# Kernel tuning notes

Measured on AMD Instinct MI355X. Metric: run time of the kernel, lower is better.

The kernel has to match this reference:

```python
import jax, jax.numpy as jnp
import numpy as np

LOCAL_RADIUS = 5


def setup_inputs() -> dict:
    key = jax.random.key(0)
    k1, k2, k3 = jax.random.split(key, 3)
    B, K, C, H = 4, 4096, 256, 128
    x = jax.random.normal(k1, (B, K, C), dtype=jnp.float32)
    W1 = jax.random.normal(k2, (C, H), dtype=jnp.float32) * (1.0 / np.sqrt(C))
    b1 = jnp.zeros((H,), dtype=jnp.float32)
    W2 = jax.random.normal(k3, (H, 1), dtype=jnp.float32) * (1.0 / np.sqrt(H))
    b2 = jnp.zeros((1,), dtype=jnp.float32)
    return {"x": x, "W1": W1, "b1": b1, "W2": W2, "b2": b2}


def reference(x, W1, b1, W2, b2):
    # x: [B, k, C]. The MLP score for column j is independent of the row i,
    # so compute it once per token instead of per (i, window) as in the torch loop.
    B, k, C = x.shape
    s = (jnp.tanh(x @ W1 + b1) @ W2 + b2)[..., 0]  # [B, k]
    idx = jnp.arange(k)
    band = (jnp.abs(idx[:, None] - idx[None, :]) <= LOCAL_RADIUS)  # [k, k]
    # Outside the band the original leaves scores at 0.0 (not -inf), so
    # out-of-window positions still contribute exp(0)=1 to the softmax.
    scores = jnp.where(band[None, :, :], s[:, None, :], jnp.float32(0.0))  # [B, k, k]
    weights = jax.nn.softmax(scores, axis=-1)  # [B, k, k]
    weighted = jnp.einsum('bij,bjc->bic', weights, x)  # [B, k, C]
    return weighted, weights
```

## Files before the change

### kernel.cpp

```cpp
#include <hip/hip_runtime.h>
#include <math.h>

#define B_ 4
#define K_ 4096
#define C_ 256
#define H_ 128
#define RAD 5

typedef float floatx4 __attribute__((ext_vector_type(4)));


__global__ __launch_bounds__(128) void score_kernel(
    const float* __restrict__ x, const float* __restrict__ W1,
    const float* __restrict__ b1, const float* __restrict__ W2,
    const float* __restrict__ b2, float* __restrict__ s_out)
{
    const int tid = threadIdx.x;
    const int t0 = blockIdx.x * 8;
    const float* xr[8];
    #pragma unroll
    for (int t = 0; t < 8; ++t) xr[t] = x + (size_t)(t0 + t) * C_;

    float acc[8];
    float binit = b1[tid];
    #pragma unroll
    for (int t = 0; t < 8; ++t) acc[t] = binit;

    for (int c = 0; c < C_; c += 4) {
        float w0 = W1[(c + 0) * H_ + tid];
        float w1 = W1[(c + 1) * H_ + tid];
        float w2 = W1[(c + 2) * H_ + tid];
        float w3 = W1[(c + 3) * H_ + tid];
        #pragma unroll
        for (int t = 0; t < 8; ++t) {
            floatx4 xv = *(const floatx4*)&xr[t][c];
            acc[t] = fmaf(xv.x, w0, acc[t]);
            acc[t] = fmaf(xv.y, w1, acc[t]);
            acc[t] = fmaf(xv.z, w2, acc[t]);
            acc[t] = fmaf(xv.w, w3, acc[t]);
        }
    }

    __shared__ float red[2][8];
    float w2v = W2[tid];
    #pragma unroll
    for (int t = 0; t < 8; ++t) {
        float p = tanhf(acc[t]) * w2v;
        #pragma unroll
        for (int off = 32; off > 0; off >>= 1) p += __shfl_down(p, off);
        if ((tid & 63) == 0) red[tid >> 6][t] = p;
    }
    __syncthreads();
    if (tid < 8) s_out[t0 + tid] = red[0][tid] + red[1][tid] + b2[0];
}

__global__ __launch_bounds__(256) void colsum_partial(
    const float* __restrict__ x, float* __restrict__ partial)
{
    const int tid = threadIdx.x;
    const int blk = blockIdx.x;
    const float* base = x + (size_t)blk * 32 * C_ + tid;
    float a0 = 0.f, a1 = 0.f, a2 = 0.f, a3 = 0.f;
    #pragma unroll
    for (int kk = 0; kk < 32; kk += 4) {
        a0 += base[(size_t)(kk + 0) * C_];
        a1 += base[(size_t)(kk + 1) * C_];
        a2 += base[(size_t)(kk + 2) * C_];
        a3 += base[(size_t)(kk + 3) * C_];
    }
    partial[(size_t)blk * C_ + tid] = (a0 + a1) + (a2 + a3);
}

__global__ __launch_bounds__(256) void colsum_final(
    const float* __restrict__ partial, float* __restrict__ Ssum)
{
    const int tid = threadIdx.x;
    const int b = blockIdx.x;
    float acc = 0.f;
    for (int chunk = 0; chunk < 128; ++chunk)
        acc += partial[(size_t)(b * 128 + chunk) * C_ + tid];
    Ssum[b * C_ + tid] = acc;
}

__global__ __launch_bounds__(256) void attn_kernel(
    const float* __restrict__ x, const float* __restrict__ s,
    const float* __restrict__ Ssum, float* __restrict__ out)
{
    const int tid = threadIdx.x;
    const int blk = blockIdx.x;
    const int b = blk >> 12;
    const int i = blk & (K_ - 1);

    __shared__ float wb[2 * RAD + 1];
    __shared__ float woff_s;
    __shared__ int j0_s, j1_s;

    if (tid == 0) {
        int j0 = i - RAD; if (j0 < 0) j0 = 0;
        int j1 = i + RAD; if (j1 > K_ - 1) j1 = K_ - 1;
        int nb = j1 - j0 + 1;
        float sv[2 * RAD + 1];
        float m = 0.f;
        const float* srow = s + b * K_;
        for (int jj = 0; jj < nb; ++jj) {
            float v = srow[j0 + jj];
            sv[jj] = v;
            m = fmaxf(m, v);
        }
        float e0 = expf(-m);
        float D = (float)(K_ - nb) * e0;
        for (int jj = 0; jj < nb; ++jj) { float e = expf(sv[jj] - m); sv[jj] = e; D += e; }
        float inv = 1.0f / D;
        for (int jj = 0; jj < nb; ++jj) wb[jj] = sv[jj] * inv;
        woff_s = e0 * inv;
        j0_s = j0; j1_s = j1;
    }
    __syncthreads();
    const float woff = woff_s;
    const int j0 = j0_s, j1 = j1_s;

    floatx4* wrow4 = (floatx4*)(out + (size_t)B_ * K_ * C_ + (size_t)blk * K_);
    #pragma unroll
    for (int q = 0; q < 4; ++q) {
        const int f = tid + 256 * q;
        const int jb = f * 4;
        floatx4 v = { woff, woff, woff, woff };
        if (jb + 3 >= j0 && jb <= j1) {
            if (jb + 0 >= j0 && jb + 0 <= j1) v.x = wb[jb + 0 - j0];
            if (jb + 1 >= j0 && jb + 1 <= j1) v.y = wb[jb + 1 - j0];
            if (jb + 2 >= j0 && jb + 2 <= j1) v.z = wb[jb + 2 - j0];
            if (jb + 3 >= j0 && jb + 3 <= j1) v.w = wb[jb + 3 - j0];
        }
        __builtin_nontemporal_store(v, wrow4 + f);
    }

    {
        float acc = woff * Ssum[b * C_ + tid];
        const float* xb = x + ((size_t)b * K_) * C_ + tid;
        for (int j = j0; j <= j1; ++j)
            acc = fmaf(wb[j - j0] - woff, xb[(size_t)j * C_], acc);
        __builtin_nontemporal_store(acc, out + (size_t)blk * C_ + tid);
    }
}

extern "C" void kernel_launch(void* const* d_in, const int* in_sizes, int n_in,
                              void* d_out, int out_size, void* d_ws, size_t ws_size,
                              hipStream_t stream) {
    const float* x  = (const float*)d_in[0];
    const float* W1 = (const float*)d_in[1];
    const float* b1 = (const float*)d_in[2];
    const float* W2 = (const float*)d_in[3];
    const float* b2 = (const float*)d_in[4];
    float* out = (float*)d_out;

    float* ws   = (float*)d_ws;
    float* s    = ws;
    float* Ssum = ws + B_ * K_;
    float* partial = out + (size_t)B_ * K_ * C_;

    score_kernel  <<<B_ * K_ / 8, 128, 0, stream>>>(x, W1, b1, W2, b2, s);
    colsum_partial<<<B_ * 128,    256, 0, stream>>>(x, partial);
    colsum_final  <<<B_,          256, 0, stream>>>(partial, Ssum);
    attn_kernel   <<<B_ * K_,     256, 0, stream>>>(x, s, Ssum, out);
}
```

Baseline: 390.9 us.

## Process eight rows per attention block with shared-memory x window

The attention kernel now handles eight consecutive rows per block. It loads the overlapping x window and scores into shared memory once and computes the eight softmaxes in parallel. This reuses neighbouring x rows across output rows and cuts block count and per-block setup. Stores switch from nontemporal to regular writes, which may change cache behaviour for the large weights output.

Measured after the change: 379.8 us. 2.8% less time.

```diff
diff --git a/kernel.cpp b/kernel.cpp
--- a/kernel.cpp
+++ b/kernel.cpp
@@ -6,6 +6,7 @@
 #define C_ 256
 #define H_ 128
 #define RAD 5
+#define ROWS 8
 
 typedef float floatx4 __attribute__((ext_vector_type(4)));
 
@@ -88,58 +89,75 @@
 {
     const int tid = threadIdx.x;
     const int blk = blockIdx.x;
-    const int b = blk >> 12;
-    const int i = blk & (K_ - 1);
+    const int b  = blk >> 9;
+    const int i0 = (blk & 511) * ROWS;
 
-    __shared__ float wb[2 * RAD + 1];
-    __shared__ float woff_s;
-    __shared__ int j0_s, j1_s;
+    const int j0t = max(0, i0 - RAD);
+    const int j1t = min(K_ - 1, i0 + ROWS - 1 + RAD);
+    const int ntok = j1t - j0t + 1;
 
-    if (tid == 0) {
-        int j0 = i - RAD; if (j0 < 0) j0 = 0;
-        int j1 = i + RAD; if (j1 > K_ - 1) j1 = K_ - 1;
-        int nb = j1 - j0 + 1;
-        float sv[2 * RAD + 1];
+    __shared__ float xs[ROWS + 2 * RAD][C_];
+    __shared__ float sb[ROWS + 2 * RAD];
+    __shared__ float wb[ROWS][2 * RAD + 1];
+    __shared__ float woff[ROWS];
+
+    if (tid < ntok) sb[tid] = s[b * K_ + j0t + tid];
+    const floatx4* xsrc = (const floatx4*)(x + ((size_t)b * K_ + j0t) * C_);
+    floatx4* xdst = (floatx4*)&xs[0][0];
+    for (int f = tid; f < ntok * (C_ / 4); f += 256) xdst[f] = xsrc[f];
+    __syncthreads();
+
+    if (tid < ROWS) {
+        const int i = i0 + tid;
+        const int j0 = max(0, i - RAD), j1 = min(K_ - 1, i + RAD);
+        const int nb = j1 - j0 + 1;
         float m = 0.f;
-        const float* srow = s + b * K_;
-        for (int jj = 0; jj < nb; ++jj) {
-            float v = srow[j0 + jj];
-            sv[jj] = v;
-            m = fmaxf(m, v);
-        }
+        for (int j = j0; j <= j1; ++j) m = fmaxf(m, sb[j - j0t]);
         float e0 = expf(-m);
         float D = (float)(K_ - nb) * e0;
-        for (int jj = 0; jj < nb; ++jj) { float e = expf(sv[jj] - m); sv[jj] = e; D += e; }
+        for (int j = j0; j <= j1; ++j) {
+            float e = expf(sb[j - j0t] - m);
+            wb[tid][j - j0] = e;
+            D += e;
+        }
         float inv = 1.0f / D;
-        for (int jj = 0; jj < nb; ++jj) wb[jj] = sv[jj] * inv;
-        woff_s = e0 * inv;
-        j0_s = j0; j1_s = j1;
+        for (int jj = 0; jj < nb; ++jj) wb[tid][jj] *= inv;
+        woff[tid] = e0 * inv;
     }
     __syncthreads();
-    const float woff = woff_s;
-    const int j0 = j0_s, j1 = j1_s;
 
-    floatx4* wrow4 = (floatx4*)(out + (size_t)B_ * K_ * C_ + (size_t)blk * K_);
+    const float sc = Ssum[b * C_ + tid];
+
     #pragma unroll
-    for (int q = 0; q < 4; ++q) {
-        const int f = tid + 256 * q;
-        const int jb = f * 4;
-        floatx4 v = { woff, woff, woff, woff };
-        if (jb + 3 >= j0 && jb <= j1) {
-            if (jb + 0 >= j0 && jb + 0 <= j1) v.x = wb[jb + 0 - j0];
-            if (jb + 1 >= j0 && jb + 1 <= j1) v.y = wb[jb + 1 - j0];
-            if (jb + 2 >= j0 && jb + 2 <= j1) v.z = wb[jb + 2 - j0];
-            if (jb + 3 >= j0 && jb + 3 <= j1) v.w = wb[jb + 3 - j0];
+    for (int r = 0; r < ROWS; ++r) {
+        const int i = i0 + r;
+        const int j0 = max(0, i - RAD), j1 = min(K_ - 1, i + RAD);
+        const float wo = woff[r];
+        floatx4* wrow4 = (floatx4*)(out + (size_t)B_ * K_ * C_ + ((size_t)b * K_ + i) * K_);
+        #pragma unroll
+        for (int q = 0; q < 4; ++q) {
+            const int f = tid + 256 * q;
+            const int jb = f * 4;
+            floatx4 v = { wo, wo, wo, wo };
+            if (jb + 3 >= j0 && jb <= j1) {
+                if (jb + 0 >= j0 && jb + 0 <= j1) v.x = wb[r][jb + 0 - j0];
+                if (jb + 1 >= j0 && jb + 1 <= j1) v.y = wb[r][jb + 1 - j0];
+                if (jb + 2 >= j0 && jb + 2 <= j1) v.z = wb[r][jb + 2 - j0];
+                if (jb + 3 >= j0 && jb + 3 <= j1) v.w = wb[r][jb + 3 - j0];
+            }
+            wrow4[f] = v;
         }
-        __builtin_nontemporal_store(v, wrow4 + f);
     }
 
-    {
-        float acc = woff * Ssum[b * C_ + tid];
-        const float* xb = x + ((size_t)b * K_) * C_ + tid;
+    #pragma unroll
+    for (int r = 0; r < ROWS; ++r) {
+        const int i = i0 + r;
+        const int j0 = max(0, i - RAD), j1 = min(K_ - 1, i + RAD);
+        const float wo = woff[r];
+        float acc = wo * sc;
         for (int j = j0; j <= j1; ++j)
-            acc = fmaf(wb[j - j0] - woff, xb[(size_t)j * C_], acc);
-        __builtin_nontemporal_store(acc, out + (size_t)blk * C_ + tid);
+            acc = fmaf(wb[r][j - j0] - wo, xs[j - j0t][tid], acc);
+        out[((size_t)b * K_ + i) * C_ + tid] = acc;
     }
 }
 
@@ -158,8 +176,8 @@
     float* Ssum = ws + B_ * K_;
     float* partial = out + (size_t)B_ * K_ * C_;
 
-    score_kernel  <<<B_ * K_ / 8, 128, 0, stream>>>(x, W1, b1, W2, b2, s);
-    colsum_partial<<<B_ * 128,    256, 0, stream>>>(x, partial);
-    colsum_final  <<<B_,          256, 0, stream>>>(partial, Ssum);
-    attn_kernel   <<<B_ * K_,     256, 0, stream>>>(x, s, Ssum, out);
+    score_kernel  <<<B_ * K_ / 8,    128, 0, stream>>>(x, W1, b1, W2, b2, s);
+    colsum_partial<<<B_ * 128,       256, 0, stream>>>(x, partial);
+    colsum_final  <<<B_,             256, 0, stream>>>(partial, Ssum);
+    attn_kernel   <<<B_ * K_ / ROWS, 256, 0, stream>>>(x, s, Ssum, out);
 }
```

## Precompute per-row softmax params in separate kernel, slim the store kernel

Applied to the files above, without the earlier changes.

The single-thread serial softmax per block is moved into a new params_kernel that computes each row's band weights and off-band weight in parallel, one thread per row, and writes them to the workspace. The store kernel now just loads 12 parameters into shared memory, does an unrolled fixed-length band accumulation, and writes the outputs. The colsum partial buffer moves from the output region into the workspace. This removes the serialized thread-0 prologue from the bandwidth-bound main kernel, at the cost of one extra launch and a small params round trip. The weighted output store also switches from nontemporal to a normal store.

After: 380.3 us. 1.03x faster.

```diff
diff --git a/kernel.cpp b/kernel.cpp
--- a/kernel.cpp
+++ b/kernel.cpp
@@ -6,6 +6,8 @@
 #define C_ 256
 #define H_ 128
 #define RAD 5
+#define NB (2 * RAD + 1)
+#define PSTRIDE 12
 
 typedef float floatx4 __attribute__((ext_vector_type(4)));
 
@@ -82,64 +84,79 @@
     Ssum[b * C_ + tid] = acc;
 }
 
-__global__ __launch_bounds__(256) void attn_kernel(
-    const float* __restrict__ x, const float* __restrict__ s,
+__global__ __launch_bounds__(256) void params_kernel(
+    const float* __restrict__ s, float* __restrict__ params)
+{
+    const int row = blockIdx.x * 256 + threadIdx.x;
+    const int b = row >> 12;
+    const int i = row & (K_ - 1);
+    const int j0 = max(0, i - RAD), j1 = min(K_ - 1, i + RAD);
+    const int nb = j1 - j0 + 1;
+    const float* srow = s + b * K_;
+
+    float sv[NB];
+    float m = 0.f;
+    #pragma unroll
+    for (int jj = 0; jj < NB; ++jj) {
+        float v = (jj < nb) ? srow[j0 + jj] : 0.f;
+        sv[jj] = v;
+        if (jj < nb) m = fmaxf(m, v);
+    }
+    float e0 = expf(-m);
+    float D = (float)(K_ - nb) * e0;
+    float* pp = params + (size_t)row * PSTRIDE;
+    #pragma unroll
+    for (int jj = 0; jj < NB; ++jj) {
+        float e = expf(sv[jj] - m);
+        if (jj < nb) D += e;
+        sv[jj] = e;
+    }
+    float inv = 1.0f / D;
+    #pragma unroll
+    for (int jj = 0; jj < NB; ++jj) pp[jj] = sv[jj] * inv;
+    pp[11] = e0 * inv;
+}
+
+__global__ __launch_bounds__(256) void store_kernel(
+    const float* __restrict__ x, const float* __restrict__ params,
     const float* __restrict__ Ssum, float* __restrict__ out)
 {
     const int tid = threadIdx.x;
-    const int blk = blockIdx.x;
-    const int b = blk >> 12;
-    const int i = blk & (K_ - 1);
+    const int row = blockIdx.x;
+    const int b = row >> 12;
+    const int i = row & (K_ - 1);
+    const int j0 = max(0, i - RAD), j1 = min(K_ - 1, i + RAD);
+    const int nb = j1 - j0 + 1;
 
-    __shared__ float wb[2 * RAD + 1];
-    __shared__ float woff_s;
-    __shared__ int j0_s, j1_s;
+    __shared__ float wbs[PSTRIDE];
+    if (tid < PSTRIDE) wbs[tid] = params[(size_t)row * PSTRIDE + tid];
+    __syncthreads();
+    const float woff = wbs[11];
 
-    if (tid == 0) {
-        int j0 = i - RAD; if (j0 < 0) j0 = 0;
-        int j1 = i + RAD; if (j1 > K_ - 1) j1 = K_ - 1;
-        int nb = j1 - j0 + 1;
-        float sv[2 * RAD + 1];
-        float m = 0.f;
-        const float* srow = s + b * K_;
-        for (int jj = 0; jj < nb; ++jj) {
-            float v = srow[j0 + jj];
-            sv[jj] = v;
-            m = fmaxf(m, v);
+    {
+        float acc = woff * Ssum[b * C_ + tid];
+        const float* xb = x + ((size_t)b * K_ + j0) * C_ + tid;
+        #pragma unroll
+        for (int jj = 0; jj < NB; ++jj) {
+            if (jj < nb)
+                acc = fmaf(wbs[jj] - woff, xb[(size_t)jj * C_], acc);
         }
-        float e0 = expf(-m);
-        float D = (float)(K_ - nb) * e0;
-        for (int jj = 0; jj < nb; ++jj) { float e = expf(sv[jj] - m); sv[jj] = e; D += e; }
-        float inv = 1.0f / D;
-        for (int jj = 0; jj < nb; ++jj) wb[jj] = sv[jj] * inv;
-        woff_s = e0 * inv;
-        j0_s = j0; j1_s = j1;
+        out[(size_t)row * C_ + tid] = acc;
     }
-    __syncthreads();
-    const float woff = woff_s;
-    const int j0 = j0_s, j1 = j1_s;
 
-    floatx4* wrow4 = (floatx4*)(out + (size_t)B_ * K_ * C_ + (size_t)blk * K_);
+    floatx4* wrow4 = (floatx4*)(out + (size_t)B_ * K_ * C_ + (size_t)row * K_);
     #pragma unroll
     for (int q = 0; q < 4; ++q) {
         const int f = tid + 256 * q;
         const int jb = f * 4;
         floatx4 v = { woff, woff, woff, woff };
         if (jb + 3 >= j0 && jb <= j1) {
-            if (jb + 0 >= j0 && jb + 0 <= j1) v.x = wb[jb + 0 - j0];
-            if (jb + 1 >= j0 && jb + 1 <= j1) v.y = wb[jb + 1 - j0];
-            if (jb + 2 >= j0 && jb + 2 <= j1) v.z = wb[jb + 2 - j0];
-            if (jb + 3 >= j0 && jb + 3 <= j1) v.w = wb[jb + 3 - j0];
+            if (jb + 0 >= j0 && jb + 0 <= j1) v.x = wbs[jb + 0 - j0];
+            if (jb + 1 >= j0 && jb + 1 <= j1) v.y = wbs[jb + 1 - j0];
+            if (jb + 2 >= j0 && jb + 2 <= j1) v.z = wbs[jb + 2 - j0];
+            if (jb + 3 >= j0 && jb + 3 <= j1) v.w = wbs[jb + 3 - j0];
         }
         __builtin_nontemporal_store(v, wrow4 + f);
-    }
-
-    {
-        float acc = woff * Ssum[b * C_ + tid];
-        const float* xb = x + ((size_t)b * K_) * C_ + tid;
-        for (int j = j0; j <= j1; ++j)
-            acc = fmaf(wb[j - j0] - woff, xb[(size_t)j * C_], acc);
-        __builtin_nontemporal_store(acc, out + (size_t)blk * C_ + tid);
     }
 }
 
@@ -153,13 +170,15 @@
     const float* b2 = (const float*)d_in[4];
     float* out = (float*)d_out;
 
-    float* ws   = (float*)d_ws;
-    float* s    = ws;
-    float* Ssum = ws + B_ * K_;
-    float* partial = out + (size_t)B_ * K_ * C_;
+    float* ws      = (float*)d_ws;
+    float* s       = ws;
+    float* Ssum    = ws + 16384;
+    float* partial = ws + 17408;
+    float* params  = ws + 148480;
 
-    score_kernel  <<<B_ * K_ / 8, 128, 0, stream>>>(x, W1, b1, W2, b2, s);
-    colsum_partial<<<B_ * 128,    256, 0, stream>>>(x, partial);
-    colsum_final  <<<B_,          256, 0, stream>>>(partial, Ssum);
-    attn_kernel   <<<B_ * K_,     256, 0, stream>>>(x, s, Ssum, out);
+    score_kernel  <<<B_ * K_ / 8,  128, 0, stream>>>(x, W1, b1, W2, b2, s);
+    colsum_partial<<<B_ * 128,     256, 0, stream>>>(x, partial);
+    colsum_final  <<<B_,           256, 0, stream>>>(partial, Ssum);
+    params_kernel <<<B_ * K_ / 256,256, 0, stream>>>(s, params);
+    store_kernel  <<<B_ * K_,      256, 0, stream>>>(x, params, Ssum, out);
 }
```
